# Performance work log

Measured on AMD Instinct MI355X. Metric: run time of the kernel, lower is better.

## Reference

```python
import jax, jax.numpy as jnp
import numpy as np

B, LI, LT = 1, 2048, 256
H, NH, HD, MLP = 1024, 16, 64, 4096
L = LI + LT


def _make_pe():
    pos = jnp.arange(L, dtype=jnp.float32)[:, None]
    omega = 1.0 / (10000.0 ** (jnp.arange(0, HD, 2, dtype=jnp.float32) / HD))  # [HD/2]
    ang = pos * omega[None, :]                                                 # [L, HD/2]
    cos, sin = jnp.cos(ang), jnp.sin(ang)
    rot = jnp.stack([jnp.stack([cos, -sin], -1), jnp.stack([sin, cos], -1)], -2)  # [L, HD/2, 2, 2]
    return rot[None, None].astype(jnp.float32)                                 # [1,1,L,HD/2,2,2]


def setup_inputs() -> dict:
    key = jax.random.key(0)
    ks = jax.random.split(key, 20)
    w = lambda k, s: jax.random.normal(k, s, jnp.float32) * 0.02
    return {
        'img': jax.random.normal(ks[0], (B, LI, H), jnp.float32),
        'txt': jax.random.normal(ks[1], (B, LT, H), jnp.float32),
        'pe': _make_pe(),
        'vec': jax.random.normal(ks[2], (B, H), jnp.float32),
        'img_mod_w': w(ks[3], (H, 6 * H)), 'img_mod_b': w(ks[4], (6 * H,)),
        'txt_mod_w': w(ks[5], (H, 6 * H)), 'txt_mod_b': w(ks[6], (6 * H,)),
        'img_qkv_w': w(ks[7], (H, 3 * H)), 'img_qkv_b': w(ks[8], (3 * H,)),
        'img_q_scale': jnp.ones((HD,), jnp.float32), 'img_k_scale': jnp.ones((HD,), jnp.float32),
        'img_proj_w': w(ks[9], (H, H)), 'img_proj_b': w(ks[10], (H,)),
        'txt_qkv_w': w(ks[11], (H, 3 * H)), 'txt_qkv_b': w(ks[12], (3 * H,)),
        'txt_q_scale': jnp.ones((HD,), jnp.float32), 'txt_k_scale': jnp.ones((HD,), jnp.float32),
        'mlp_w1': w(ks[13], (H, MLP)), 'mlp_b1': w(ks[14], (MLP,)),
        'mlp_w2': w(ks[15], (MLP, H)), 'mlp_b2': w(ks[16], (H,)),
    }


def _ln(x):  # LayerNorm, no affine, eps=1e-6
    m = jnp.mean(x, -1, keepdims=True)
    v = jnp.mean((x - m) ** 2, -1, keepdims=True)
    return (x - m) * jax.lax.rsqrt(v + 1e-6)


def _rms(x, scale):  # QKNorm RMSNorm, eps=1e-6, learned per-dim scale
    return x * jax.lax.rsqrt(jnp.mean(x * x, -1, keepdims=True) + 1e-6) * scale


def _qkv_heads(x, w, b):
    b_, l_, _ = x.shape
    qkv = (jnp.einsum('bld,de->ble', x, w) + b).reshape(b_, l_, 3, NH, HD)
    qkv = jnp.transpose(qkv, (2, 0, 3, 1, 4))  # [3,B,H,L,D]
    return qkv[0], qkv[1], qkv[2]


def _rope(x, pe):
    xr = x.reshape(x.shape[:-1] + (HD // 2, 1, 2))  # [B,H,L,HD/2,1,2]
    out = pe[..., 0] * xr[..., 0] + pe[..., 1] * xr[..., 1]
    return out.reshape(x.shape)


def reference(img, txt, pe, vec, img_mod_w, img_mod_b, txt_mod_w, txt_mod_b,
              img_qkv_w, img_qkv_b, img_q_scale, img_k_scale, img_proj_w, img_proj_b,
              txt_qkv_w, txt_qkv_b, txt_q_scale, txt_k_scale,
              mlp_w1, mlp_b1, mlp_w2, mlp_b2):
    sv = jax.nn.silu(vec)
    imod = (jnp.einsum('bd,de->be', sv, img_mod_w) + img_mod_b)[:, None, :]
    i_shift1, i_scale1, i_gate1, i_shift2, i_scale2, i_gate2 = jnp.split(imod, 6, -1)
    tmod = (jnp.einsum('bd,de->be', sv, txt_mod_w) + txt_mod_b)[:, None, :]
    t_shift1, t_scale1 = jnp.split(tmod, 6, -1)[0], jnp.split(tmod, 6, -1)[1]

    img_m = (1 + i_scale1) * _ln(img) + i_shift1
    iq, ik, iv = _qkv_heads(img_m, img_qkv_w, img_qkv_b)
    iq, ik = _rms(iq, img_q_scale), _rms(ik, img_k_scale)

    txt_m = (1 + t_scale1) * _ln(txt) + t_shift1
    tq, tk, tv = _qkv_heads(txt_m, txt_qkv_w, txt_qkv_b)
    tq, tk = _rms(tq, txt_q_scale), _rms(tk, txt_k_scale)

    q = _rope(jnp.concatenate([tq, iq], 2), pe)
    k = _rope(jnp.concatenate([tk, ik], 2), pe)
    v = jnp.concatenate([tv, iv], 2)

    scores = jnp.einsum('bhqd,bhkd->bhqk', q, k) / np.float32(np.sqrt(HD))
    attn = jnp.einsum('bhqk,bhkd->bhqd', jax.nn.softmax(scores, -1), v)
    attn = jnp.transpose(attn, (0, 2, 1, 3)).reshape(attn.shape[0], L, NH * HD)

    img_attn = attn[:, txt.shape[1]:]
    img = img + i_gate1 * (jnp.einsum('bld,de->ble', img_attn, img_proj_w) + img_proj_b)
    h = (1 + i_scale2) * _ln(img) + i_shift2
    h = jax.nn.gelu(jnp.einsum('bld,de->ble', h, mlp_w1) + mlp_b1, approximate=True)
    h = jnp.einsum('bld,de->ble', h, mlp_w2) + mlp_b2
    return img + i_gate2 * h
```

## Files before the change

kernel.cpp:

```cpp
#include <hip/hip_runtime.h>
#include <cstdint>
#include <cstddef>

typedef unsigned short u16;
typedef __attribute__((ext_vector_type(8))) short bf16x8;
typedef __attribute__((ext_vector_type(4))) float f32x4;

#define AS1 __attribute__((address_space(1)))
#define AS3 __attribute__((address_space(3)))
#define GLDS16(g, s) __builtin_amdgcn_global_load_lds((const AS1 void*)(g), (AS3 void*)(s), 16, 0, 0)

__device__ inline u16 f2bf(float f) {
  union { float f; unsigned u; } c; c.f = f;
  unsigned r = c.u + 0x7fffu + ((c.u >> 16) & 1u);
  return (u16)(r >> 16);
}
__device__ inline float bf2f(u16 s) {
  union { unsigned u; float f; } c; c.u = ((unsigned)s) << 16;
  return c.f;
}
__device__ inline unsigned cvt_pk_bf16(float a, float b) {
  unsigned r;
  asm("v_cvt_pk_bf16_f32 %0, %1, %2" : "=v"(r) : "v"(a), "v"(b));
  return r;
}

__global__ __launch_bounds__(256)
void wconv_t(const float* __restrict__ W, u16* __restrict__ Wt, int K, int N) {
  __shared__ float tile[32][33];
  const int tx = threadIdx.x, ty = threadIdx.y;
  const int n0 = blockIdx.x * 32, k0 = blockIdx.y * 32;
#pragma unroll
  for (int i = 0; i < 4; ++i)
    tile[ty + i * 8][tx] = W[(size_t)(k0 + ty + i * 8) * N + n0 + tx];
  __syncthreads();
#pragma unroll
  for (int i = 0; i < 4; ++i)
    Wt[(size_t)(n0 + ty + i * 8) * K + k0 + tx] = f2bf(tile[tx][ty + i * 8]);
}

__global__ __launch_bounds__(256)
void silu_kernel(const float* __restrict__ vec, float* __restrict__ sv) {
  int i = blockIdx.x * 256 + threadIdx.x;
  float x = vec[i];
  sv[i] = x / (1.f + __expf(-x));
}

__global__ __launch_bounds__(256)
void modinit(const float* __restrict__ imb, const float* __restrict__ tmb, float* __restrict__ mod) {
  int i = blockIdx.x * 256 + threadIdx.x;
  mod[i] = (i < 6144) ? imb[i] : tmb[i - 6144];
}

__global__ __launch_bounds__(256)
void modgemv(const float* __restrict__ sv, const float* __restrict__ imw,
             const float* __restrict__ tmw, float* __restrict__ mod) {
  __shared__ float s[128];
  const int t = threadIdx.x;
  const int c = blockIdx.x * 256 + t;
  const int kc = blockIdx.y * 128;
  if (t < 128) s[t] = sv[kc + t];
  __syncthreads();
  const float* W; int col;
  if (c < 6144) { W = imw; col = c; } else { W = tmw; col = c - 6144; }
  float acc = 0.f;
#pragma unroll 8
  for (int k = 0; k < 128; ++k) acc += s[k] * W[(size_t)(kc + k) * 6144 + col];
  atomicAdd(&mod[c], acc);
}

__global__ __launch_bounds__(256)
void ln_mod(const float* __restrict__ x, const float* __restrict__ shift,
            const float* __restrict__ scale, u16* __restrict__ out) {
  const int row = blockIdx.x, t = threadIdx.x;
  const float* xr = x + (size_t)row * 1024;
  float v[4], s = 0.f, sq = 0.f;
#pragma unroll
  for (int i = 0; i < 4; ++i) { v[i] = xr[t + i * 256]; s += v[i]; sq += v[i] * v[i]; }
#pragma unroll
  for (int o = 32; o; o >>= 1) { s += __shfl_down(s, o); sq += __shfl_down(sq, o); }
  __shared__ float ls[8];
  if ((t & 63) == 0) { ls[t >> 6] = s; ls[4 + (t >> 6)] = sq; }
  __syncthreads();
  s = ls[0] + ls[1] + ls[2] + ls[3];
  sq = ls[4] + ls[5] + ls[6] + ls[7];
  const float mean = s * (1.f / 1024.f);
  const float var = sq * (1.f / 1024.f) - mean * mean;
  const float rstd = rsqrtf(var + 1e-6f);
#pragma unroll
  for (int i = 0; i < 4; ++i) {
    int c = t + i * 256;
    float xn = (v[i] - mean) * rstd;
    out[(size_t)row * 1024 + c] = f2bf((1.f + scale[c]) * xn + shift[c]);
  }
}

template <int EPI, int BN>
__global__ __launch_bounds__(256, 3)
void gemm_bt(const u16* __restrict__ A, const u16* __restrict__ Bt,
             int M, int N, int K,
             const float* __restrict__ bias, const float* __restrict__ gate,
             const float* __restrict__ resid, void* __restrict__ Cout) {
  constexpr int NF = BN / 32;
  __shared__ u16 smA[128 * 32];
  __shared__ u16 smB[BN * 32];
  const int t = threadIdx.x;
  const int w = t >> 6, l = t & 63;
  const int lr = l & 15, lg = l >> 4;
  const int m0 = blockIdx.x * 128, n0 = blockIdx.y * BN;
  const int wm = (w >> 1) * 64, wn = (w & 1) * (BN / 2);
  f32x4 acc[4][NF] = {};
  const int c0 = w * 64 + l, c1 = c0 + 256;
  const int r0 = c0 >> 2, cb0 = (c0 & 3) << 3;
  const int r1 = c1 >> 2, cb1 = (c1 & 3) << 3;
  const int nk = K >> 5;
  for (int kt = 0; kt < nk; ++kt) {
    const int k0 = kt << 5;
    GLDS16(A + (size_t)(m0 + r0) * K + k0 + cb0, smA + (w * 64) * 8);
    GLDS16(A + (size_t)(m0 + r1) * K + k0 + cb1, smA + (256 + w * 64) * 8);
    GLDS16(Bt + (size_t)(n0 + r0) * K + k0 + cb0, smB + (w * 64) * 8);
    if constexpr (BN == 128)
      GLDS16(Bt + (size_t)(n0 + r1) * K + k0 + cb1, smB + (256 + w * 64) * 8);
    __syncthreads();
    bf16x8 af[4], bfr[NF];
#pragma unroll
    for (int m = 0; m < 4; ++m)
      af[m] = *(const bf16x8*)(smA + (wm + m * 16 + lr) * 32 + lg * 8);
#pragma unroll
    for (int n = 0; n < NF; ++n)
      bfr[n] = *(const bf16x8*)(smB + (wn + n * 16 + lr) * 32 + lg * 8);
#pragma unroll
    for (int m = 0; m < 4; ++m)
#pragma unroll
      for (int n = 0; n < NF; ++n)
        acc[m][n] = __builtin_amdgcn_mfma_f32_16x16x32_bf16(af[m], bfr[n], acc[m][n], 0, 0, 0);
    __syncthreads();
  }
#pragma unroll
  for (int m = 0; m < 4; ++m) {
    const int row = m0 + wm + m * 16 + lg * 4;
#pragma unroll
    for (int n = 0; n < NF; ++n) {
      const int col = n0 + wn + n * 16 + lr;
#pragma unroll
      for (int i = 0; i < 4; ++i) {
        float v = acc[m][n][i];
        size_t idx = (size_t)(row + i) * N + col;
        if constexpr (EPI == 0) {
          ((u16*)Cout)[idx] = f2bf(v + bias[col]);
        } else if constexpr (EPI == 2) {
          float cc = v + bias[col];
          float u = 0.7978845608f * (cc + 0.044715f * cc * cc * cc);
          float e = __expf(2.f * u);
          float th = 1.f - 2.f / (e + 1.f);
          ((u16*)Cout)[idx] = f2bf(0.5f * cc * (1.f + th));
        } else {
          ((float*)Cout)[idx] = resid[idx] + gate[col] * (v + bias[col]);
        }
      }
    }
  }
}

__global__ __launch_bounds__(256)
void qk_post(const u16* __restrict__ qkv_txt, const u16* __restrict__ qkv_img,
             const float* __restrict__ pe,
             const float* __restrict__ iq_s, const float* __restrict__ ik_s,
             const float* __restrict__ tq_s, const float* __restrict__ tk_s,
             u16* __restrict__ Q, u16* __restrict__ K) {
  const int d = threadIdx.x;
  const int pos = blockIdx.x * 4 + threadIdx.y;
  const int h = blockIdx.y;
  const u16* src; int r; const float *qs, *ks;
  if (pos < 256) { src = qkv_txt; r = pos; qs = tq_s; ks = tk_s; }
  else           { src = qkv_img; r = pos - 256; qs = iq_s; ks = ik_s; }
  float q = bf2f(src[(size_t)r * 3072 + h * 64 + d]);
  float k = bf2f(src[(size_t)r * 3072 + 1024 + h * 64 + d]);
  float qsq = q * q, ksq = k * k;
#pragma unroll
  for (int o = 32; o; o >>= 1) { qsq += __shfl_xor(qsq, o); ksq += __shfl_xor(ksq, o); }
  q *= rsqrtf(qsq * (1.f / 64.f) + 1e-6f) * qs[d];
  k *= rsqrtf(ksq * (1.f / 64.f) + 1e-6f) * ks[d];
  const int p = d >> 1, odd = d & 1;
  const float* pp = pe + (((size_t)pos * 32 + p) * 2 + odd) * 2;
  float qp = __shfl_xor(q, 1), kp = __shfl_xor(k, 1);
  float qe = odd ? qp : q, qo = odd ? q : qp;
  float ke = odd ? kp : k, ko = odd ? k : kp;
  float rq = pp[0] * qe + pp[1] * qo;
  float rk = pp[0] * ke + pp[1] * ko;
  size_t oidx = ((size_t)h * 2304 + pos) * 64 + d;
  Q[oidx] = f2bf(rq * 0.125f);
  K[oidx] = f2bf(rk);
}

__global__ __launch_bounds__(512)
void v_transpose(const u16* __restrict__ qkv_txt, const u16* __restrict__ qkv_img,
                 u16* __restrict__ Vt) {
  __shared__ float tile[64][65];
  const int tx = threadIdx.x, ty = threadIdx.y;
  const int p0 = blockIdx.x * 64, h = blockIdx.y;
#pragma unroll
  for (int i = 0; i < 8; ++i) {
    int pos = p0 + ty + i * 8;
    const u16* src; int r;
    if (pos < 256) { src = qkv_txt; r = pos; } else { src = qkv_img; r = pos - 256; }
    tile[ty + i * 8][tx] = bf2f(src[(size_t)r * 3072 + 2048 + h * 64 + tx]);
  }
  __syncthreads();
#pragma unroll
  for (int i = 0; i < 8; ++i) {
    int d = ty + i * 8;
    Vt[((size_t)h * 64 + d) * 2304 + p0 + tx] = f2bf(tile[tx][d]);
  }
}

__global__ __launch_bounds__(256, 3)
void attn_kernel(const u16* __restrict__ Q, const u16* __restrict__ Kb,
                 const u16* __restrict__ Vt,
                 float* __restrict__ Opart, float* __restrict__ ml) {
  __shared__ u16 smK[2][64 * 64];
  __shared__ u16 smV[2][64 * 64];
  __shared__ u16 smP[4 * 16 * 72];
  const int t = threadIdx.x, w = t >> 6, l = t & 63;
  const int lr = l & 15, lg = l >> 4;
  const int qt = blockIdx.x, h = blockIdx.y, sp = blockIdx.z;
  const int j0 = sp * 18;
  const u16* Qp = Q + ((size_t)h * 2304 + qt * 64 + w * 16 + lr) * 64;
  const bf16x8 qf0 = *(const bf16x8*)(Qp + lg * 8);
  const bf16x8 qf1 = *(const bf16x8*)(Qp + 32 + lg * 8);
  const u16* Kbase = Kb + (size_t)h * 2304 * 64;
  const u16* Vbase = Vt + (size_t)h * 64 * 2304;
  f32x4 accO[4] = {};
  float mrun = -1e30f, lrun = 0.f;
  u16* myP = smP + w * (16 * 72);

  const int c0 = w * 64 + l, c1 = c0 + 256;
  const int kr0 = c0 >> 3, ks0 = ((c0 & 7) ^ (kr0 & 7)) * 8;
  const int kr1 = c1 >> 3, ks1 = ((c1 & 7) ^ (kr1 & 7)) * 8;

  auto stage = [&](int j, int b) {
    const u16* gK = Kbase + (size_t)j * 64 * 64;
    GLDS16(gK + (size_t)kr0 * 64 + ks0, smK[b] + (w * 64) * 8);
    GLDS16(gK + (size_t)kr1 * 64 + ks1, smK[b] + (256 + w * 64) * 8);
    GLDS16(Vbase + (size_t)kr0 * 2304 + j * 64 + ks0, smV[b] + (w * 64) * 8);
    GLDS16(Vbase + (size_t)kr1 * 2304 + j * 64 + ks1, smV[b] + (256 + w * 64) * 8);
  };

  stage(j0, 0);
  for (int jj = 0; jj < 18; ++jj) {
    const int b = jj & 1;
    if (jj < 17) {
      stage(j0 + jj + 1, b ^ 1);
      asm volatile("s_waitcnt vmcnt(4)" ::: "memory");
    } else {
      asm volatile("s_waitcnt vmcnt(0)" ::: "memory");
    }
    __builtin_amdgcn_s_barrier();
    asm volatile("" ::: "memory");

    f32x4 sf[4];
    __builtin_amdgcn_s_setprio(1);
#pragma unroll
    for (int n = 0; n < 4; ++n) {
      const int row = n * 16 + lr, sw = row & 7;
      bf16x8 kf0 = *(const bf16x8*)(smK[b] + row * 64 + ((lg ^ sw) << 3));
      bf16x8 kf1 = *(const bf16x8*)(smK[b] + row * 64 + (((lg + 4) ^ sw) << 3));
      f32x4 z = {};
      z = __builtin_amdgcn_mfma_f32_16x16x32_bf16(kf0, qf0, z, 0, 0, 0);
      z = __builtin_amdgcn_mfma_f32_16x16x32_bf16(kf1, qf1, z, 0, 0, 0);
      sf[n] = z;
    }
    __builtin_amdgcn_s_setprio(0);

    float t0 = fmaxf(fmaxf(sf[0][0], sf[0][1]), fmaxf(sf[0][2], sf[0][3]));
    float t1 = fmaxf(fmaxf(sf[1][0], sf[1][1]), fmaxf(sf[1][2], sf[1][3]));
    float t2 = fmaxf(fmaxf(sf[2][0], sf[2][1]), fmaxf(sf[2][2], sf[2][3]));
    float t3 = fmaxf(fmaxf(sf[3][0], sf[3][1]), fmaxf(sf[3][2], sf[3][3]));
    float mx = fmaxf(fmaxf(t0, t1), fmaxf(t2, t3));
    mx = fmaxf(mx, __shfl_xor(mx, 16));
    mx = fmaxf(mx, __shfl_xor(mx, 32));
    const float mnew = fmaxf(mrun, mx);
    const float corr = __expf(mrun - mnew);
    mrun = mnew;

    float p[4][4];
    float s0 = 0.f, s1 = 0.f, s2 = 0.f, s3 = 0.f;
#pragma unroll
    for (int n = 0; n < 4; ++n) {
      p[n][0] = __expf(sf[n][0] - mnew);
      p[n][1] = __expf(sf[n][1] - mnew);
      p[n][2] = __expf(sf[n][2] - mnew);
      p[n][3] = __expf(sf[n][3] - mnew);
    }
    s0 = (p[0][0] + p[0][1]) + (p[0][2] + p[0][3]);
    s1 = (p[1][0] + p[1][1]) + (p[1][2] + p[1][3]);
    s2 = (p[2][0] + p[2][1]) + (p[2][2] + p[2][3]);
    s3 = (p[3][0] + p[3][1]) + (p[3][2] + p[3][3]);
    float rs = (s0 + s1) + (s2 + s3);
    rs += __shfl_xor(rs, 16);
    rs += __shfl_xor(rs, 32);
    lrun = lrun * corr + rs;

#pragma unroll
    for (int n = 0; n < 4; ++n) {
      *(unsigned*)(myP + lr * 72 + n * 16 + lg * 4)     = cvt_pk_bf16(p[n][0], p[n][1]);
      *(unsigned*)(myP + lr * 72 + n * 16 + lg * 4 + 2) = cvt_pk_bf16(p[n][2], p[n][3]);
    }

    float cb[4];
#pragma unroll
    for (int i = 0; i < 4; ++i) cb[i] = __shfl(corr, lg * 4 + i);
#pragma unroll
    for (int nd = 0; nd < 4; ++nd)
#pragma unroll
      for (int i = 0; i < 4; ++i) accO[nd][i] *= cb[i];

    __builtin_amdgcn_s_setprio(1);
#pragma unroll
    for (int c = 0; c < 2; ++c) {
      bf16x8 pf = *(const bf16x8*)(myP + lr * 72 + c * 32 + lg * 8);
#pragma unroll
      for (int nd = 0; nd < 4; ++nd) {
        const int row = nd * 16 + lr, sw = row & 7;
        bf16x8 vf = *(const bf16x8*)(smV[b] + row * 64 + (((c * 4 + lg) ^ sw) << 3));
        accO[nd] = __builtin_amdgcn_mfma_f32_16x16x32_bf16(pf, vf, accO[nd], 0, 0, 0);
      }
    }
    __builtin_amdgcn_s_setprio(0);
    asm volatile("" ::: "memory");
    __builtin_amdgcn_s_barrier();
  }

  float* Op = Opart + (((size_t)(sp * 16 + h) * 2304) + qt * 64) * 64;
#pragma unroll
  for (int nd = 0; nd < 4; ++nd)
#pragma unroll
    for (int i = 0; i < 4; ++i)
      Op[(size_t)(w * 16 + lg * 4 + i) * 64 + nd * 16 + lr] = accO[nd][i];
  if (lg == 0) {
    size_t mi = ((size_t)(sp * 16 + h) * 2304 + qt * 64 + w * 16 + lr) * 2;
    ml[mi] = mrun;
    ml[mi + 1] = lrun;
  }
}

__global__ __launch_bounds__(256)
void attn_combine(const float* __restrict__ Opart, const float* __restrict__ ml,
                  u16* __restrict__ outb) {
  int idx = blockIdx.x * 256 + threadIdx.x;
  int q = idx >> 10, c = idx & 1023;
  int h = c >> 6, d = c & 63;
  size_t i0 = (size_t)h * 2304 + q;
  size_t i1 = (size_t)(16 + h) * 2304 + q;
  float m0 = ml[i0 * 2], l0 = ml[i0 * 2 + 1];
  float m1 = ml[i1 * 2], l1 = ml[i1 * 2 + 1];
  float M = fmaxf(m0, m1);
  float w0 = __expf(m0 - M), w1 = __expf(m1 - M);
  float a0 = Opart[i0 * 64 + d], a1 = Opart[i1 * 64 + d];
  float num = w0 * a0 + w1 * a1;
  float den = w0 * l0 + w1 * l1;
  outb[(size_t)q * 1024 + c] = f2bf(num / den);
}

extern "C" void kernel_launch(void* const* d_in, const int* in_sizes, int n_in,
                              void* d_out, int out_size, void* d_ws, size_t ws_size,
                              hipStream_t stream) {
  const float* img         = (const float*)d_in[0];
  const float* txt         = (const float*)d_in[1];
  const float* pe          = (const float*)d_in[2];
  const float* vec         = (const float*)d_in[3];
  const float* img_mod_w   = (const float*)d_in[4];
  const float* img_mod_b   = (const float*)d_in[5];
  const float* txt_mod_w   = (const float*)d_in[6];
  const float* txt_mod_b   = (const float*)d_in[7];
  const float* img_qkv_w   = (const float*)d_in[8];
  const float* img_qkv_b   = (const float*)d_in[9];
  const float* img_q_scale = (const float*)d_in[10];
  const float* img_k_scale = (const float*)d_in[11];
  const float* img_proj_w  = (const float*)d_in[12];
  const float* img_proj_b  = (const float*)d_in[13];
  const float* txt_qkv_w   = (const float*)d_in[14];
  const float* txt_qkv_b   = (const float*)d_in[15];
  const float* txt_q_scale = (const float*)d_in[16];
  const float* txt_k_scale = (const float*)d_in[17];
  const float* mlp_w1      = (const float*)d_in[18];
  const float* mlp_b1      = (const float*)d_in[19];
  const float* mlp_w2      = (const float*)d_in[20];
  const float* mlp_b2      = (const float*)d_in[21];
  (void)in_sizes; (void)n_in; (void)out_size; (void)ws_size;

  char* ws = (char*)d_ws;
  size_t off = 0;
  auto alloc = [&](size_t bytes) -> void* {
    void* p = ws + off;
    off += (bytes + 255) & ~(size_t)255;
    return p;
  };
  float* sv     = (float*)alloc(1024 * 4);
  float* mod    = (float*)alloc(8192 * 4);
  u16* qkv_img  = (u16*)alloc((size_t)2048 * 3072 * 2);
  u16* qkv_txt  = (u16*)alloc((size_t)256 * 3072 * 2);
  u16* img_m    = (u16*)alloc((size_t)2048 * 1024 * 2);
  u16* txt_m    = (u16*)alloc((size_t)256 * 1024 * 2);
  float* Opart  = (float*)qkv_img;
  float* mlbuf  = (float*)alloc((size_t)2 * 16 * 2304 * 2 * 4);
  u16* wt_iqkv  = (u16*)alloc((size_t)3072 * 1024 * 2);
  u16* wt_tqkv  = (u16*)alloc((size_t)3072 * 1024 * 2);
  u16* wt_proj  = (u16*)alloc((size_t)1024 * 1024 * 2);
  u16* wt_m1    = (u16*)alloc((size_t)4096 * 1024 * 2);
  u16* wt_m2    = (u16*)alloc((size_t)1024 * 4096 * 2);
  u16* Qb       = (u16*)alloc((size_t)16 * 2304 * 64 * 2);
  u16* Kb       = (u16*)alloc((size_t)16 * 2304 * 64 * 2);
  u16* Vtb      = (u16*)alloc((size_t)16 * 64 * 2304 * 2);
  u16* attnb    = (u16*)alloc((size_t)2304 * 1024 * 2);
  float* img2   = (float*)alloc((size_t)2048 * 1024 * 4);
  u16* h_in     = (u16*)alloc((size_t)2048 * 1024 * 2);
  u16* h1       = (u16*)alloc((size_t)2048 * 4096 * 2);

  const dim3 bT(32, 8);
  wconv_t<<<dim3(3072 / 32, 1024 / 32), bT, 0, stream>>>(img_qkv_w, wt_iqkv, 1024, 3072);
  wconv_t<<<dim3(3072 / 32, 1024 / 32), bT, 0, stream>>>(txt_qkv_w, wt_tqkv, 1024, 3072);
  wconv_t<<<dim3(1024 / 32, 1024 / 32), bT, 0, stream>>>(img_proj_w, wt_proj, 1024, 1024);
  wconv_t<<<dim3(4096 / 32, 1024 / 32), bT, 0, stream>>>(mlp_w1, wt_m1, 1024, 4096);
  wconv_t<<<dim3(1024 / 32, 4096 / 32), bT, 0, stream>>>(mlp_w2, wt_m2, 4096, 1024);

  silu_kernel<<<4, 256, 0, stream>>>(vec, sv);
  modinit<<<32, 256, 0, stream>>>(img_mod_b, txt_mod_b, mod);
  modgemv<<<dim3(32, 8), 256, 0, stream>>>(sv, img_mod_w, txt_mod_w, mod);

  ln_mod<<<2048, 256, 0, stream>>>(img, mod + 0, mod + 1024, img_m);
  ln_mod<<<256, 256, 0, stream>>>(txt, mod + 6144, mod + 7168, txt_m);

  gemm_bt<0, 128><<<dim3(16, 24), 256, 0, stream>>>(img_m, wt_iqkv, 2048, 3072, 1024,
                                                    img_qkv_b, nullptr, nullptr, qkv_img);
  gemm_bt<0, 128><<<dim3(2, 24), 256, 0, stream>>>(txt_m, wt_tqkv, 256, 3072, 1024,
                                                   txt_qkv_b, nullptr, nullptr, qkv_txt);

  qk_post<<<dim3(576, 16), dim3(64, 4), 0, stream>>>(qkv_txt, qkv_img, pe,
                                                     img_q_scale, img_k_scale,
                                                     txt_q_scale, txt_k_scale, Qb, Kb);
  v_transpose<<<dim3(36, 16), dim3(64, 8), 0, stream>>>(qkv_txt, qkv_img, Vtb);

  attn_kernel<<<dim3(36, 16, 2), 256, 0, stream>>>(Qb, Kb, Vtb, Opart, mlbuf);
  attn_combine<<<9216, 256, 0, stream>>>(Opart, mlbuf, attnb);

  gemm_bt<1, 64><<<dim3(16, 16), 256, 0, stream>>>(attnb + (size_t)256 * 1024, wt_proj,
                                                   2048, 1024, 1024,
                                                   img_proj_b, mod + 2048, img, img2);
  ln_mod<<<2048, 256, 0, stream>>>(img2, mod + 3072, mod + 4096, h_in);
  gemm_bt<2, 128><<<dim3(16, 32), 256, 0, stream>>>(h_in, wt_m1, 2048, 4096, 1024,
                                                    mlp_b1, nullptr, nullptr, h1);
  gemm_bt<3, 64><<<dim3(16, 16), 256, 0, stream>>>(h1, wt_m2, 2048, 1024, 4096,
                                                   mlp_b2, mod + 5120, img2, (float*)d_out);
}
```

Measured before the change: 442.5 us.

## Double-buffer GEMM LDS with swizzle, smaller tiles, and split-K for MLP down-proj

Rewrites the GEMM main loop to double-buffer the A/B tiles in LDS, prefetching the next K-slice while computing the current one, using explicit vmcnt waits and raw barriers. It also XOR-swizzles the LDS layout to reduce bank conflicts. Tile shape becomes a template parameter, so the projection GEMM uses 64x64 tiles for more blocks, and the MLP down-projection is split-K across two blocks followed by a combine kernel that applies bias, gate and residual. The cost is twice the LDS per block, which can lower occupancy, plus the extra fp32 partial-buffer traffic and one more launch for split-K.

```diff
diff --git a/kernel.cpp b/kernel.cpp
--- a/kernel.cpp
+++ b/kernel.cpp
@@ -95,49 +95,84 @@
   }
 }
 
-template <int EPI, int BN>
+template <int EPI, int BM, int BN>
 __global__ __launch_bounds__(256, 3)
 void gemm_bt(const u16* __restrict__ A, const u16* __restrict__ Bt,
-             int M, int N, int K,
+             int M, int N, int Kstride, int Kspan,
              const float* __restrict__ bias, const float* __restrict__ gate,
              const float* __restrict__ resid, void* __restrict__ Cout) {
-  constexpr int NF = BN / 32;
-  __shared__ u16 smA[128 * 32];
-  __shared__ u16 smB[BN * 32];
+  constexpr int MF = BM / 32, NF = BN / 32, L = (BM + BN) / 64;
+  __shared__ u16 smA[2][BM * 32];
+  __shared__ u16 smB[2][BN * 32];
   const int t = threadIdx.x;
   const int w = t >> 6, l = t & 63;
   const int lr = l & 15, lg = l >> 4;
-  const int m0 = blockIdx.x * 128, n0 = blockIdx.y * BN;
-  const int wm = (w >> 1) * 64, wn = (w & 1) * (BN / 2);
-  f32x4 acc[4][NF] = {};
-  const int c0 = w * 64 + l, c1 = c0 + 256;
-  const int r0 = c0 >> 2, cb0 = (c0 & 3) << 3;
-  const int r1 = c1 >> 2, cb1 = (c1 & 3) << 3;
-  const int nk = K >> 5;
+  const int m0 = blockIdx.x * BM, n0 = blockIdx.y * BN;
+  const int koff = blockIdx.z * Kspan;
+  const int wm = (w >> 1) * (BM / 2), wn = (w & 1) * (BN / 2);
+  f32x4 acc[MF][NF] = {};
+
+  const u16* gb[L];
+  int doff[L];
+  bool isA[L];
+#pragma unroll
+  for (int i = 0; i < L; ++i) {
+    int c = t + i * 256;
+    if (c < BM * 4) {
+      int row = c >> 2, ch = c & 3;
+      gb[i] = A + (size_t)(m0 + row) * Kstride + koff + ((ch ^ ((row >> 1) & 3)) << 3);
+      doff[i] = c * 8; isA[i] = true;
+    } else {
+      int cc = c - BM * 4, row = cc >> 2, ch = cc & 3;
+      gb[i] = Bt + (size_t)(n0 + row) * Kstride + koff + ((ch ^ ((row >> 1) & 3)) << 3);
+      doff[i] = cc * 8; isA[i] = false;
+    }
+  }
+  auto stage = [&](int kt, int b) {
+#pragma unroll
+    for (int i = 0; i < L; ++i)
+      GLDS16(gb[i] + (kt << 5), (isA[i] ? smA[b] : smB[b]) + doff[i]);
+  };
+
+  const int nk = Kspan >> 5;
+  stage(0, 0);
   for (int kt = 0; kt < nk; ++kt) {
-    const int k0 = kt << 5;
-    GLDS16(A + (size_t)(m0 + r0) * K + k0 + cb0, smA + (w * 64) * 8);
-    GLDS16(A + (size_t)(m0 + r1) * K + k0 + cb1, smA + (256 + w * 64) * 8);
-    GLDS16(Bt + (size_t)(n0 + r0) * K + k0 + cb0, smB + (w * 64) * 8);
-    if constexpr (BN == 128)
-      GLDS16(Bt + (size_t)(n0 + r1) * K + k0 + cb1, smB + (256 + w * 64) * 8);
-    __syncthreads();
-    bf16x8 af[4], bfr[NF];
-#pragma unroll
-    for (int m = 0; m < 4; ++m)
-      af[m] = *(const bf16x8*)(smA + (wm + m * 16 + lr) * 32 + lg * 8);
-#pragma unroll
-    for (int n = 0; n < NF; ++n)
-      bfr[n] = *(const bf16x8*)(smB + (wn + n * 16 + lr) * 32 + lg * 8);
-#pragma unroll
-    for (int m = 0; m < 4; ++m)
+    const int b = kt & 1;
+    if (kt < nk - 1) {
+      stage(kt + 1, b ^ 1);
+      if constexpr (L == 4)      asm volatile("s_waitcnt vmcnt(4)" ::: "memory");
+      else if constexpr (L == 3) asm volatile("s_waitcnt vmcnt(3)" ::: "memory");
+      else                       asm volatile("s_waitcnt vmcnt(2)" ::: "memory");
+    } else {
+      asm volatile("s_waitcnt vmcnt(0)" ::: "memory");
+    }
+    __builtin_amdgcn_s_barrier();
+    asm volatile("" ::: "memory");
+
+    bf16x8 af[MF], bfr[NF];
+#pragma unroll
+    for (int m = 0; m < MF; ++m) {
+      int row = wm + m * 16 + lr;
+      af[m] = *(const bf16x8*)(smA[b] + row * 32 + ((lg ^ ((row >> 1) & 3)) << 3));
+    }
+#pragma unroll
+    for (int n = 0; n < NF; ++n) {
+      int row = wn + n * 16 + lr;
+      bfr[n] = *(const bf16x8*)(smB[b] + row * 32 + ((lg ^ ((row >> 1) & 3)) << 3));
+    }
+    __builtin_amdgcn_s_setprio(1);
+#pragma unroll
+    for (int m = 0; m < MF; ++m)
 #pragma unroll
       for (int n = 0; n < NF; ++n)
         acc[m][n] = __builtin_amdgcn_mfma_f32_16x16x32_bf16(af[m], bfr[n], acc[m][n], 0, 0, 0);
-    __syncthreads();
-  }
-#pragma unroll
-  for (int m = 0; m < 4; ++m) {
+    __builtin_amdgcn_s_setprio(0);
+    asm volatile("" ::: "memory");
+    __builtin_amdgcn_s_barrier();
+  }
+
+#pragma unroll
+  for (int m = 0; m < MF; ++m) {
     const int row = m0 + wm + m * 16 + lg * 4;
 #pragma unroll
     for (int n = 0; n < NF; ++n) {
@@ -154,12 +189,24 @@
           float e = __expf(2.f * u);
           float th = 1.f - 2.f / (e + 1.f);
           ((u16*)Cout)[idx] = f2bf(0.5f * cc * (1.f + th));
+        } else if constexpr (EPI == 4) {
+          ((float*)Cout)[(size_t)blockIdx.z * M * N + idx] = v;
         } else {
           ((float*)Cout)[idx] = resid[idx] + gate[col] * (v + bias[col]);
         }
       }
     }
   }
+}
+
+__global__ __launch_bounds__(256)
+void combine2(const float* __restrict__ part, const float* __restrict__ bias,
+              const float* __restrict__ gate, const float* __restrict__ resid,
+              float* __restrict__ out) {
+  size_t idx = (size_t)blockIdx.x * 256 + threadIdx.x;
+  int col = (int)(idx & 1023);
+  float v = part[idx] + part[(size_t)2048 * 1024 + idx] + bias[col];
+  out[idx] = resid[idx] + gate[col] * v;
 }
 
 __global__ __launch_bounds__(256)
@@ -284,7 +331,6 @@
     mrun = mnew;
 
     float p[4][4];
-    float s0 = 0.f, s1 = 0.f, s2 = 0.f, s3 = 0.f;
 #pragma unroll
     for (int n = 0; n < 4; ++n) {
       p[n][0] = __expf(sf[n][0] - mnew);
@@ -292,10 +338,10 @@
       p[n][2] = __expf(sf[n][2] - mnew);
       p[n][3] = __expf(sf[n][3] - mnew);
     }
-    s0 = (p[0][0] + p[0][1]) + (p[0][2] + p[0][3]);
-    s1 = (p[1][0] + p[1][1]) + (p[1][2] + p[1][3]);
-    s2 = (p[2][0] + p[2][1]) + (p[2][2] + p[2][3]);
-    s3 = (p[3][0] + p[3][1]) + (p[3][2] + p[3][3]);
+    float s0 = (p[0][0] + p[0][1]) + (p[0][2] + p[0][3]);
+    float s1 = (p[1][0] + p[1][1]) + (p[1][2] + p[1][3]);
+    float s2 = (p[2][0] + p[2][1]) + (p[2][2] + p[2][3]);
+    float s3 = (p[3][0] + p[3][1]) + (p[3][2] + p[3][3]);
     float rs = (s0 + s1) + (s2 + s3);
     rs += __shfl_xor(rs, 16);
     rs += __shfl_xor(rs, 32);
@@ -403,6 +449,7 @@
   u16* img_m    = (u16*)alloc((size_t)2048 * 1024 * 2);
   u16* txt_m    = (u16*)alloc((size_t)256 * 1024 * 2);
   float* Opart  = (float*)qkv_img;
+  float* pml2   = (float*)qkv_img;
   float* mlbuf  = (float*)alloc((size_t)2 * 16 * 2304 * 2 * 4);
   u16* wt_iqkv  = (u16*)alloc((size_t)3072 * 1024 * 2);
   u16* wt_tqkv  = (u16*)alloc((size_t)3072 * 1024 * 2);
@@ -431,10 +478,10 @@
   ln_mod<<<2048, 256, 0, stream>>>(img, mod + 0, mod + 1024, img_m);
   ln_mod<<<256, 256, 0, stream>>>(txt, mod + 6144, mod + 7168, txt_m);
 
-  gemm_bt<0, 128><<<dim3(16, 24), 256, 0, stream>>>(img_m, wt_iqkv, 2048, 3072, 1024,
-                                                    img_qkv_b, nullptr, nullptr, qkv_img);
-  gemm_bt<0, 128><<<dim3(2, 24), 256, 0, stream>>>(txt_m, wt_tqkv, 256, 3072, 1024,
-                                                   txt_qkv_b, nullptr, nullptr, qkv_txt);
+  gemm_bt<0, 128, 128><<<dim3(16, 24), 256, 0, stream>>>(img_m, wt_iqkv, 2048, 3072, 1024, 1024,
+                                                         img_qkv_b, nullptr, nullptr, qkv_img);
+  gemm_bt<0, 128, 128><<<dim3(2, 24), 256, 0, stream>>>(txt_m, wt_tqkv, 256, 3072, 1024, 1024,
+                                                        txt_qkv_b, nullptr, nullptr, qkv_txt);
 
   qk_post<<<dim3(576, 16), dim3(64, 4), 0, stream>>>(qkv_txt, qkv_img, pe,
                                                      img_q_scale, img_k_scale,
@@ -444,12 +491,13 @@
   attn_kernel<<<dim3(36, 16, 2), 256, 0, stream>>>(Qb, Kb, Vtb, Opart, mlbuf);
   attn_combine<<<9216, 256, 0, stream>>>(Opart, mlbuf, attnb);
 
-  gemm_bt<1, 64><<<dim3(16, 16), 256, 0, stream>>>(attnb + (size_t)256 * 1024, wt_proj,
-                                                   2048, 1024, 1024,
-                                                   img_proj_b, mod + 2048, img, img2);
+  gemm_bt<1, 64, 64><<<dim3(32, 16), 256, 0, stream>>>(attnb + (size_t)256 * 1024, wt_proj,
+                                                       2048, 1024, 1024, 1024,
+                                                       img_proj_b, mod + 2048, img, img2);
   ln_mod<<<2048, 256, 0, stream>>>(img2, mod + 3072, mod + 4096, h_in);
-  gemm_bt<2, 128><<<dim3(16, 32), 256, 0, stream>>>(h_in, wt_m1, 2048, 4096, 1024,
-                                                    mlp_b1, nullptr, nullptr, h1);
-  gemm_bt<3, 64><<<dim3(16, 16), 256, 0, stream>>>(h1, wt_m2, 2048, 1024, 4096,
-                                                   mlp_b2, mod + 5120, img2, (float*)d_out);
-}
+  gemm_bt<2, 128, 128><<<dim3(16, 32), 256, 0, stream>>>(h_in, wt_m1, 2048, 4096, 1024, 1024,
+                                                         mlp_b1, nullptr, nullptr, h1);
+  gemm_bt<4, 64, 64><<<dim3(32, 16, 2), 256, 0, stream>>>(h1, wt_m2, 2048, 1024, 4096, 2048,
+                                                          nullptr, nullptr, nullptr, pml2);
+  combine2<<<8192, 256, 0, stream>>>(pml2, mlp_b2, mod + 5120, img2, (float*)d_out);
+}
```

New measurement: 411.9 us. 1.07x faster.
